# Performance work log

Hardware: AMD Instinct MI355X
Metric: run time of the kernel (lower is better)

## Reference

```python
import jax, jax.numpy as jnp
import numpy as np

B, S, H, NH = 4, 2048, 256, 8
EPS = 1e-5


def setup_inputs() -> dict:
    key = jax.random.key(0)
    ks = jax.random.split(key, 12)
    p = lambda k, shape: (jax.random.normal(k, shape, jnp.float32) * 0.02)
    return {
        "x": jax.random.normal(ks[0], (B, S, H), jnp.float32),
        "lengths": jax.random.randint(ks[1], (B,), 0, S).astype(jnp.int32),
        "atten_in": jnp.zeros((1,), jnp.float32),
        "Wq": p(ks[2], (H, H)), "bq": jnp.zeros((H,), jnp.float32),
        "Wk": p(ks[3], (H, H)), "bk": jnp.zeros((H,), jnp.float32),
        "Wv": p(ks[4], (H, H)), "bv": jnp.zeros((H,), jnp.float32),
        "W1": p(ks[5], (H, H)), "b1": jnp.zeros((H,), jnp.float32),
        "W2": p(ks[6], (H, H)), "b2": jnp.zeros((H,), jnp.float32),
        "g1": jnp.ones((H,), jnp.float32), "beta1": jnp.zeros((H,), jnp.float32),
        "g2": jnp.ones((H,), jnp.float32), "beta2": jnp.zeros((H,), jnp.float32),
    }


def _layer_norm(x, g, b):
    mu = x.mean(-1, keepdims=True)
    var = ((x - mu) ** 2).mean(-1, keepdims=True)
    return (x - mu) / jnp.sqrt(var + EPS) * g + b


def reference(x, lengths, atten_in, Wq, bq, Wk, bk, Wv, bv, W1, b1, W2, b2, g1, beta1, g2, beta2):
    Bx, Sx, Hx = x.shape
    hd = Hx // NH
    # QKV projections, split heads -> [B, NH, S, hd]
    q = (x @ Wq + bq).reshape(Bx, Sx, NH, hd).transpose(0, 2, 1, 3)
    k = (x @ Wk + bk).reshape(Bx, Sx, NH, hd).transpose(0, 2, 1, 3)
    v = (x @ Wv + bv).reshape(Bx, Sx, NH, hd).transpose(0, 2, 1, 3)
    # NOTE: original scales by sqrt(hidden_size), not sqrt(head_dim)
    scores = jnp.einsum('bhqd,bhkd->bhqk', q, k) / np.sqrt(Hx).astype(np.float32)
    pos = jnp.arange(Sx)
    causal = pos[:, None] >= pos[None, :]                     # [S, S]
    row_ok = pos[None, :] < lengths[:, None]                  # [B, S]: mask query rows >= length
    head_ok = jnp.arange(NH)[None, :] < lengths[:, None]      # [B, NH]: original loop masks heads >= length
    mask = causal[None, None] & row_ok[:, None, :, None] & head_ok[:, :, None, None]
    neg = jnp.finfo(scores.dtype).min
    logits = jnp.where(mask, scores, neg)
    atten = jax.nn.softmax(logits, axis=-1)
    # original: masked_fill((atten > 0) == False, 0) -> fully masked rows (NaN in torch) become 0
    atten = jnp.where(mask, atten, 0.0)
    row_valid = mask.any(-1, keepdims=True)
    atten = jnp.where(row_valid, atten, 0.0)
    out = jnp.einsum('bhqk,bhkd->bhqd', atten, v).transpose(0, 2, 1, 3).reshape(Bx, Sx, Hx)
    atten_mean = atten.mean(axis=1)  # [B, S, S], detached in original
    out_1 = x + out  # dropout p=0 / eval mode -> identity
    out_1_norm = _layer_norm(out_1, g1, beta1)
    ff = jax.nn.gelu(out_1_norm @ W1 + b1, approximate=False) @ W2 + b2
    y_prim = _layer_norm(out_1_norm + ff, g2, beta2)
    return (y_prim, lengths, atten_mean)
```

## Files before the change

### kernel.cpp

```cpp
#include <hip/hip_runtime.h>
#include <math.h>

#define BB 4
#define SS 2048
#define HH 256
#define NHH 8
#define EPSV 1e-5f
#define NC 8
#define CHW (SS/NC)
#define NCO 4
#define QPRE 0.09016844005556021f

#if __has_builtin(__builtin_amdgcn_exp2f)
#define EXP2F(x) __builtin_amdgcn_exp2f(x)
#else
#define EXP2F(x) __expf((x) * 0.6931471805599453f)
#endif

typedef unsigned short ushortT;
typedef __attribute__((ext_vector_type(8))) short bf16x8;
typedef __attribute__((ext_vector_type(4))) float f32x4;

__device__ inline ushortT f2bf(float f) {
    union { float f; unsigned int u; } x; x.f = f;
    unsigned int r = x.u + 0x7FFFu + ((x.u >> 16) & 1u);
    return (ushortT)(r >> 16);
}
__device__ inline ushortT f2bf_rz(float f) {
    union { float f; unsigned int u; } x; x.f = f;
    return (ushortT)(x.u >> 16);
}
__device__ inline float bf2f(ushortT u) {
    union { unsigned int i; float f; } x; x.i = ((unsigned int)u) << 16;
    return x.f;
}

__global__ __launch_bounds__(256) void prep(const int* __restrict__ L,
        float* __restrict__ out_len,
        const float* __restrict__ Wa, const float* __restrict__ Wb,
        const float* __restrict__ Wc, const float* __restrict__ Wd,
        const float* __restrict__ We, ushortT* __restrict__ Wtb) {
    const int wb = blockIdx.x;
    if (wb == 0 && threadIdx.x < BB) out_len[threadIdx.x] = (float)L[threadIdx.x];
    const int z = wb >> 6;
    const int rem = wb & 63;
    const int k0 = (rem >> 3) << 5, n0 = (rem & 7) << 5;
    const float* W = (z == 0) ? Wa : (z == 1) ? Wb : (z == 2) ? Wc : (z == 3) ? Wd : We;
    __shared__ float tile[32][33];
    const int t = threadIdx.x;
    const int r = t >> 3, c4 = (t & 7) << 2;
    float4 v = *(const float4*)(W + (size_t)(k0 + r) * HH + n0 + c4);
    tile[r][c4+0] = v.x; tile[r][c4+1] = v.y; tile[r][c4+2] = v.z; tile[r][c4+3] = v.w;
    __syncthreads();
    ushort4 o;
    o.x = f2bf(tile[c4+0][r]); o.y = f2bf(tile[c4+1][r]);
    o.z = f2bf(tile[c4+2][r]); o.w = f2bf(tile[c4+3][r]);
    *(ushort4*)(Wtb + (size_t)z * 65536 + (size_t)(n0 + r) * HH + k0 + c4) = o;
}

__global__ __launch_bounds__(256) void gemm_qkv(const float* __restrict__ X,
        const ushortT* __restrict__ Wtb,
        const float* __restrict__ bq, const float* __restrict__ bk,
        const float* __restrict__ bv,
        ushortT* __restrict__ Qb, ushortT* __restrict__ Kb,
        ushortT* __restrict__ Vt) {
    __shared__ ushortT As[64][264];
    __shared__ ushortT Ws[64][264];
    const int wsel = blockIdx.y >> 2;
    const int n0 = (blockIdx.y & 3) << 6;
    const ushortT* Wt = Wtb + (size_t)wsel * 65536;
    const float* bias = (wsel == 0) ? bq : (wsel == 1) ? bk : bv;
    const int tid = threadIdx.x;
    const int m0 = blockIdx.x << 6;
    #pragma unroll
    for (int t = 0; t < 8; ++t) {
        const int f = t * 256 + tid;
        const int r = f >> 5;
        const int cc = (f & 31) << 3;
        const float* xrow = X + (size_t)(m0 + r) * HH + cc;
        float4 v0 = *(const float4*)xrow;
        float4 v1 = *(const float4*)(xrow + 4);
        bf16x8 o;
        o[0] = (short)f2bf(v0.x); o[1] = (short)f2bf(v0.y);
        o[2] = (short)f2bf(v0.z); o[3] = (short)f2bf(v0.w);
        o[4] = (short)f2bf(v1.x); o[5] = (short)f2bf(v1.y);
        o[6] = (short)f2bf(v1.z); o[7] = (short)f2bf(v1.w);
        *(bf16x8*)&As[r][cc] = o;
        *(bf16x8*)&Ws[r][cc] = *(const bf16x8*)(Wt + (size_t)(n0 + r) * HH + cc);
    }
    __syncthreads();
    const int w = tid >> 6, lane = tid & 63;
    const int lg = lane >> 4, lc = lane & 15;
    const int wr = (w & 1) << 5, wc = (w >> 1) << 5;
    f32x4 acc[2][2];
    const f32x4 z4 = {0.f, 0.f, 0.f, 0.f};
    acc[0][0] = z4; acc[0][1] = z4; acc[1][0] = z4; acc[1][1] = z4;
    #pragma unroll
    for (int k0 = 0; k0 < 256; k0 += 32) {
        bf16x8 a0 = *(const bf16x8*)&As[wr + lc][k0 + lg*8];
        bf16x8 a1 = *(const bf16x8*)&As[wr + 16 + lc][k0 + lg*8];
        bf16x8 b0 = *(const bf16x8*)&Ws[wc + lc][k0 + lg*8];
        bf16x8 b1 = *(const bf16x8*)&Ws[wc + 16 + lc][k0 + lg*8];
        acc[0][0] = __builtin_amdgcn_mfma_f32_16x16x32_bf16(a0, b0, acc[0][0], 0, 0, 0);
        acc[0][1] = __builtin_amdgcn_mfma_f32_16x16x32_bf16(a0, b1, acc[0][1], 0, 0, 0);
        acc[1][0] = __builtin_amdgcn_mfma_f32_16x16x32_bf16(a1, b0, acc[1][0], 0, 0, 0);
        acc[1][1] = __builtin_amdgcn_mfma_f32_16x16x32_bf16(a1, b1, acc[1][1], 0, 0, 0);
    }
    ushortT* Out = (wsel == 0) ? Qb : Kb;
    #pragma unroll
    for (int RH = 0; RH < 2; ++RH)
        #pragma unroll
        for (int CH = 0; CH < 2; ++CH) {
            const int col = n0 + wc + CH*16 + lc;
            const float bvv = bias[col];
            float v[4];
            #pragma unroll
            for (int r = 0; r < 4; ++r) {
                v[r] = acc[RH][CH][r] + bvv;
                if (wsel == 0) v[r] *= QPRE;
            }
            if (wsel < 2) {
                #pragma unroll
                for (int r = 0; r < 4; ++r) {
                    const int row = m0 + wr + RH*16 + lg*4 + r;
                    Out[(size_t)row * HH + col] = f2bf(v[r]);
                }
            } else {
                const int row0 = m0 + wr + RH*16 + lg*4;
                const int bidx = row0 >> 11, s0 = row0 & (SS - 1);
                ushort4 o;
                o.x = f2bf(v[0]); o.y = f2bf(v[1]); o.z = f2bf(v[2]); o.w = f2bf(v[3]);
                *(ushort4*)(Vt + ((size_t)(bidx * HH + col)) * SS + s0) = o;
            }
        }
}

template<int MODE>
__global__ __launch_bounds__(256) void gemm_mfma(const ushortT* __restrict__ A,
        const ushortT* __restrict__ Wt, const float* __restrict__ bias,
        void* __restrict__ Cv) {
    __shared__ ushortT As[64][264];
    __shared__ ushortT Ws[64][264];
    const int tid = threadIdx.x;
    const int m0 = blockIdx.x << 6;
    const int n0 = blockIdx.y << 6;
    #pragma unroll
    for (int t = 0; t < 8; ++t) {
        const int f = t * 256 + tid;
        const int r = f >> 5;
        const int cc = (f & 31) << 3;
        *(bf16x8*)&As[r][cc] = *(const bf16x8*)(A + (size_t)(m0 + r) * HH + cc);
        *(bf16x8*)&Ws[r][cc] = *(const bf16x8*)(Wt + (size_t)(n0 + r) * HH + cc);
    }
    __syncthreads();
    const int w = tid >> 6, lane = tid & 63;
    const int lg = lane >> 4, lc = lane & 15;
    const int wr = (w & 1) << 5, wc = (w >> 1) << 5;
    f32x4 acc[2][2];
    const f32x4 z4 = {0.f, 0.f, 0.f, 0.f};
    acc[0][0] = z4; acc[0][1] = z4; acc[1][0] = z4; acc[1][1] = z4;
    #pragma unroll
    for (int k0 = 0; k0 < 256; k0 += 32) {
        bf16x8 a0 = *(const bf16x8*)&As[wr + lc][k0 + lg*8];
        bf16x8 a1 = *(const bf16x8*)&As[wr + 16 + lc][k0 + lg*8];
        bf16x8 b0 = *(const bf16x8*)&Ws[wc + lc][k0 + lg*8];
        bf16x8 b1 = *(const bf16x8*)&Ws[wc + 16 + lc][k0 + lg*8];
        acc[0][0] = __builtin_amdgcn_mfma_f32_16x16x32_bf16(a0, b0, acc[0][0], 0, 0, 0);
        acc[0][1] = __builtin_amdgcn_mfma_f32_16x16x32_bf16(a0, b1, acc[0][1], 0, 0, 0);
        acc[1][0] = __builtin_amdgcn_mfma_f32_16x16x32_bf16(a1, b0, acc[1][0], 0, 0, 0);
        acc[1][1] = __builtin_amdgcn_mfma_f32_16x16x32_bf16(a1, b1, acc[1][1], 0, 0, 0);
    }
    #pragma unroll
    for (int RH = 0; RH < 2; ++RH)
        #pragma unroll
        for (int CH = 0; CH < 2; ++CH) {
            const int col = n0 + wc + CH*16 + lc;
            const float bv = bias[col];
            #pragma unroll
            for (int r = 0; r < 4; ++r) {
                const int row = m0 + wr + RH*16 + lg*4 + r;
                float v = acc[RH][CH][r] + bv;
                if (MODE == 2) v = 0.5f * v * (1.0f + erff(v * 0.70710678118f));
                ((ushortT*)Cv)[(size_t)row * HH + col] = f2bf(v);
            }
        }
}

__global__ __launch_bounds__(512) void ffn2_ln(const ushortT* __restrict__ A,
        const ushortT* __restrict__ W2t, const float* __restrict__ b2,
        const float* __restrict__ X1N, const float* __restrict__ g,
        const float* __restrict__ be, float* __restrict__ out) {
    __shared__ ushortT Ws[256][264];
    __shared__ ushortT As[32][264];
    __shared__ float redA[8][32];
    __shared__ float redB[8][32];
    const int tid = threadIdx.x;
    const int m0 = blockIdx.x << 5;
    #pragma unroll
    for (int t = 0; t < 16; ++t) {
        const int f = t * 512 + tid;
        const int r = f >> 5;
        const int cc = (f & 31) << 3;
        *(bf16x8*)&Ws[r][cc] = *(const bf16x8*)(W2t + (size_t)r * HH + cc);
    }
    #pragma unroll
    for (int t = 0; t < 2; ++t) {
        const int f = t * 512 + tid;
        const int r = f >> 5;
        const int cc = (f & 31) << 3;
        *(bf16x8*)&As[r][cc] = *(const bf16x8*)(A + (size_t)(m0 + r) * HH + cc);
    }
    __syncthreads();
    const int w = tid >> 6, lane = tid & 63;
    const int lg = lane >> 4, lc = lane & 15;
    const int n0 = (w >> 1) << 6;
    const int ch = (w & 1) << 5;
    f32x4 acc[2][2];
    const f32x4 z4 = {0.f, 0.f, 0.f, 0.f};
    acc[0][0] = z4; acc[0][1] = z4; acc[1][0] = z4; acc[1][1] = z4;
    #pragma unroll
    for (int k0 = 0; k0 < 256; k0 += 32) {
        bf16x8 a0 = *(const bf16x8*)&As[lc][k0 + lg*8];
        bf16x8 a1 = *(const bf16x8*)&As[16 + lc][k0 + lg*8];
        bf16x8 b0 = *(const bf16x8*)&Ws[n0 + ch + lc][k0 + lg*8];
        bf16x8 b1 = *(const bf16x8*)&Ws[n0 + ch + 16 + lc][k0 + lg*8];
        acc[0][0] = __builtin_amdgcn_mfma_f32_16x16x32_bf16(a0, b0, acc[0][0], 0, 0, 0);
        acc[0][1] = __builtin_amdgcn_mfma_f32_16x16x32_bf16(a0, b1, acc[0][1], 0, 0, 0);
        acc[1][0] = __builtin_amdgcn_mfma_f32_16x16x32_bf16(a1, b0, acc[1][0], 0, 0, 0);
        acc[1][1] = __builtin_amdgcn_mfma_f32_16x16x32_bf16(a1, b1, acc[1][1], 0, 0, 0);
    }
    float v[2][2][4];
    float rs[2][4] = {};
    #pragma unroll
    for (int RH = 0; RH < 2; ++RH)
        #pragma unroll
        for (int CH = 0; CH < 2; ++CH) {
            const int col = n0 + ch + CH*16 + lc;
            const float bv = b2[col];
            #pragma unroll
            for (int r = 0; r < 4; ++r) {
                const int row = m0 + RH*16 + lg*4 + r;
                float vv = acc[RH][CH][r] + bv + X1N[(size_t)row * HH + col];
                v[RH][CH][r] = vv;
                rs[RH][r] += vv;
            }
        }
    #pragma unroll
    for (int RH = 0; RH < 2; ++RH)
        #pragma unroll
        for (int r = 0; r < 4; ++r) {
            rs[RH][r] += __shfl_xor(rs[RH][r], 1);
            rs[RH][r] += __shfl_xor(rs[RH][r], 2);
            rs[RH][r] += __shfl_xor(rs[RH][r], 4);
            rs[RH][r] += __shfl_xor(rs[RH][r], 8);
        }
    if (lc == 0) {
        #pragma unroll
        for (int RH = 0; RH < 2; ++RH)
            #pragma unroll
            for (int r = 0; r < 4; ++r)
                redA[w][RH*16 + lg*4 + r] = rs[RH][r];
    }
    __syncthreads();
    float mu[2][4];
    #pragma unroll
    for (int RH = 0; RH < 2; ++RH)
        #pragma unroll
        for (int r = 0; r < 4; ++r) {
            const int rl = RH*16 + lg*4 + r;
            mu[RH][r] = (redA[0][rl] + redA[1][rl] + redA[2][rl] + redA[3][rl]
                       + redA[4][rl] + redA[5][rl] + redA[6][rl] + redA[7][rl])
                      * 0.00390625f;
        }
    float qs[2][4] = {};
    #pragma unroll
    for (int RH = 0; RH < 2; ++RH)
        #pragma unroll
        for (int CH = 0; CH < 2; ++CH)
            #pragma unroll
            for (int r = 0; r < 4; ++r) {
                const float d = v[RH][CH][r] - mu[RH][r];
                qs[RH][r] += d * d;
            }
    #pragma unroll
    for (int RH = 0; RH < 2; ++RH)
        #pragma unroll
        for (int r = 0; r < 4; ++r) {
            qs[RH][r] += __shfl_xor(qs[RH][r], 1);
            qs[RH][r] += __shfl_xor(qs[RH][r], 2);
            qs[RH][r] += __shfl_xor(qs[RH][r], 4);
            qs[RH][r] += __shfl_xor(qs[RH][r], 8);
        }
    if (lc == 0) {
        #pragma unroll
        for (int RH = 0; RH < 2; ++RH)
            #pragma unroll
            for (int r = 0; r < 4; ++r)
                redB[w][RH*16 + lg*4 + r] = qs[RH][r];
    }
    __syncthreads();
    #pragma unroll
    for (int RH = 0; RH < 2; ++RH)
        #pragma unroll
        for (int r = 0; r < 4; ++r) {
            const int rl = RH*16 + lg*4 + r;
            const float var = (redB[0][rl] + redB[1][rl] + redB[2][rl] + redB[3][rl]
                             + redB[4][rl] + redB[5][rl] + redB[6][rl] + redB[7][rl])
                            * 0.00390625f;
            const float rq = rsqrtf(var + EPSV);
            const int row = m0 + rl;
            #pragma unroll
            for (int CH = 0; CH < 2; ++CH) {
                const int col = n0 + ch + CH*16 + lc;
                out[(size_t)row * HH + col] =
                    (v[RH][CH][r] - mu[RH][r]) * rq * g[col] + be[col];
            }
        }
}

__global__ __launch_bounds__(512) void attn_sums(const ushortT* __restrict__ Qb,
        const ushortT* __restrict__ Kb, const int* __restrict__ lengths,
        float* __restrict__ Psum, float* __restrict__ out_mean) {
    const int b = blockIdx.z, c = blockIdx.y;
    const int i0 = (63 - blockIdx.x) << 5;
    const int len = lengths[b];
    const int tid = threadIdx.x;
    const int w = tid >> 6, lane = tid & 63;
    const int T = (i0 < len) ? ((min(i0 + 31, len - 1) >> 5) + 1) : 0;
    {
        const int zs = max(T * 32 - c * CHW, 0);
        if (zs < CHW) {
            #pragma unroll
            for (int rr = 0; rr < 4; ++rr) {
                float* mrow = out_mean + ((size_t)(b * SS + i0 + w * 4 + rr)) * SS + c * CHW;
                const int col = zs + (lane << 2);
                if (col < CHW)
                    *(float4*)(mrow + col) = make_float4(0.f, 0.f, 0.f, 0.f);
            }
        }
    }
    const int jmax = min(i0 + 31, len - 1);
    const int jstart = c * CHW;
    if (i0 >= len || jstart > jmax) return;
    const int lg = lane >> 4, lc = lane & 15;
    bf16x8 qf[2];
    #pragma unroll
    for (int RH = 0; RH < 2; ++RH)
        qf[RH] = *(const bf16x8*)(Qb + ((size_t)(b * SS + i0 + RH*16 + lc)) * HH + w*32 + lg*8);
    const f32x4 z4 = {0.f, 0.f, 0.f, 0.f};
    float lsum[2][4] = {};
    const int jend = min(jstart + CHW - 32, (jmax >> 5) << 5);
    bf16x8 kf0 = *(const bf16x8*)(Kb + ((size_t)(b * SS + jstart + lc)) * HH + w*32 + lg*8);
    bf16x8 kf1 = *(const bf16x8*)(Kb + ((size_t)(b * SS + jstart + 16 + lc)) * HH + w*32 + lg*8);
    for (int j0 = jstart; j0 <= jend; j0 += 32) {
        bf16x8 ck0 = kf0, ck1 = kf1;
        if (j0 + 32 <= jend) {
            kf0 = *(const bf16x8*)(Kb + ((size_t)(b * SS + j0 + 32 + lc)) * HH + w*32 + lg*8);
            kf1 = *(const bf16x8*)(Kb + ((size_t)(b * SS + j0 + 48 + lc)) * HH + w*32 + lg*8);
        }
        f32x4 s[2][2];
        #pragma unroll
        for (int RH = 0; RH < 2; ++RH) {
            s[RH][0] = __builtin_amdgcn_mfma_f32_16x16x32_bf16(qf[RH], ck0, z4, 0, 0, 0);
            s[RH][1] = __builtin_amdgcn_mfma_f32_16x16x32_bf16(qf[RH], ck1, z4, 0, 0, 0);
        }
        if (j0 < i0) {
            #pragma unroll
            for (int RH = 0; RH < 2; ++RH)
                #pragma unroll
                for (int r = 0; r < 4; ++r)
                    #pragma unroll
                    for (int CH = 0; CH < 2; ++CH)
                        lsum[RH][r] += EXP2F(s[RH][CH][r]);
        } else {
            #pragma unroll
            for (int RH = 0; RH < 2; ++RH)
                #pragma unroll
                for (int r = 0; r < 4; ++r) {
                    const int row = i0 + RH*16 + lg*4 + r;
                    #pragma unroll
                    for (int CH = 0; CH < 2; ++CH) {
                        const int j = j0 + CH*16 + lc;
                        lsum[RH][r] += (j <= row) ? EXP2F(s[RH][CH][r]) : 0.f;
                    }
                }
        }
    }
    #pragma unroll
    for (int RH = 0; RH < 2; ++RH)
        #pragma unroll
        for (int r = 0; r < 4; ++r) {
            float v = lsum[RH][r];
            v += __shfl_xor(v, 1); v += __shfl_xor(v, 2);
            v += __shfl_xor(v, 4); v += __shfl_xor(v, 8);
            if (lc == 0)
                Psum[((size_t)(c * BB + b) * NHH + w) * SS + i0 + RH*16 + lg*4 + r] = v;
        }
}

__global__ __launch_bounds__(512) void attn_pv(const ushortT* __restrict__ Qb,
        const ushortT* __restrict__ Kb, const ushortT* __restrict__ Vt,
        const int* __restrict__ lengths, const float* __restrict__ Psum,
        ushortT* __restrict__ OPart, float* __restrict__ out_mean) {
    __shared__ __align__(16) ushortT Pb[2][NHH][32][40];
    __shared__ float invS[NHH][32];
    const int b = blockIdx.z, cg = blockIdx.y;
    const int i0 = (63 - blockIdx.x) << 5;
    const int len = lengths[b];
    const int tid = threadIdx.x;
    const int mr = tid >> 4, mc = (tid & 15) << 1;
    float* meanrow = out_mean + ((size_t)(b * SS + i0 + mr)) * SS + mc;
    const int T = (i0 < len) ? ((min(i0 + 31, len - 1) >> 5) + 1) : 0;
    const int q = T >> 2, r = T & (NCO - 1);
    const int t0 = cg * q + min(cg, r);
    const int t1 = t0 + q + (cg < r ? 1 : 0);
    if (t0 >= t1) return;
    if (tid < NHH * 32) {
        const int hh = tid >> 5, row = i0 + (tid & 31);
        float rv = 0.f;
        if (row < len && hh < len) {
            float s = 0.f;
            const int ncv = (row >> 8) + 1;
            for (int c2 = 0; c2 < ncv; ++c2)
                s += Psum[((size_t)(c2 * BB + b) * NHH + hh) * SS + row];
            rv = (s > 0.f) ? 1.0f / s : 0.f;
        }
        invS[hh][tid & 31] = rv;
    }
    __syncthreads();
    const int w = tid >> 6, lane = tid & 63;
    const int lg = lane >> 4, lc = lane & 15;
    bf16x8 qf[2];
    #pragma unroll
    for (int RH = 0; RH < 2; ++RH)
        qf[RH] = *(const bf16x8*)(Qb + ((size_t)(b * SS + i0 + RH*16 + lc)) * HH + w*32 + lg*8);
    float invv[2][4];
    #pragma unroll
    for (int RH = 0; RH < 2; ++RH)
        #pragma unroll
        for (int r2 = 0; r2 < 4; ++r2)
            invv[RH][r2] = invS[w][RH*16 + lg*4 + r2];
    float invh8[NHH];
    #pragma unroll
    for (int hh = 0; hh < NHH; ++hh)
        invh8[hh] = invS[hh][mr] * 0.125f;
    const f32x4 z4 = {0.f, 0.f, 0.f, 0.f};
    f32x4 O[2][2];
    O[0][0] = z4; O[0][1] = z4; O[1][0] = z4; O[1][1] = z4;
    const int jstart = t0 << 5;
    bf16x8 kf0 = *(const bf16x8*)(Kb + ((size_t)(b * SS + jstart + lc)) * HH + w*32 + lg*8);
    bf16x8 kf1 = *(const bf16x8*)(Kb + ((size_t)(b * SS + jstart + 16 + lc)) * HH + w*32 + lg*8);
    bf16x8 vf0 = *(const bf16x8*)(Vt + ((size_t)(b * HH + w*32 + lc)) * SS + jstart + lg*8);
    bf16x8 vf1 = *(const bf16x8*)(Vt + ((size_t)(b * HH + w*32 + 16 + lc)) * SS + jstart + lg*8);
    for (int t = t0; t < t1; ++t) {
        const int j0 = t << 5;
        const int par = t & 1;
        bf16x8 ck0 = kf0, ck1 = kf1, cv0 = vf0, cv1 = vf1;
        if (t + 1 < t1) {
            kf0 = *(const bf16x8*)(Kb + ((size_t)(b * SS + j0 + 32 + lc)) * HH + w*32 + lg*8);
            kf1 = *(const bf16x8*)(Kb + ((size_t)(b * SS + j0 + 48 + lc)) * HH + w*32 + lg*8);
            vf0 = *(const bf16x8*)(Vt + ((size_t)(b * HH + w*32 + lc)) * SS + j0 + 32 + lg*8);
            vf1 = *(const bf16x8*)(Vt + ((size_t)(b * HH + w*32 + 16 + lc)) * SS + j0 + 32 + lg*8);
        }
        f32x4 s[2][2];
        #pragma unroll
        for (int RH = 0; RH < 2; ++RH) {
            s[RH][0] = __builtin_amdgcn_mfma_f32_16x16x32_bf16(qf[RH], ck0, z4, 0, 0, 0);
            s[RH][1] = __builtin_amdgcn_mfma_f32_16x16x32_bf16(qf[RH], ck1, z4, 0, 0, 0);
        }
        if (j0 < i0) {
            #pragma unroll
            for (int RH = 0; RH < 2; ++RH)
                #pragma unroll
                for (int CH = 0; CH < 2; ++CH)
                    #pragma unroll
                    for (int r2 = 0; r2 < 4; ++r2)
                        Pb[par][w][RH*16 + lg*4 + r2][CH*16 + lc] =
                            f2bf_rz(EXP2F(s[RH][CH][r2]));
        } else {
            #pragma unroll
            for (int RH = 0; RH < 2; ++RH)
                #pragma unroll
                for (int CH = 0; CH < 2; ++CH)
                    #pragma unroll
                    for (int r2 = 0; r2 < 4; ++r2) {
                        const int row = i0 + RH*16 + lg*4 + r2;
                        const int j = j0 + CH*16 + lc;
                        Pb[par][w][RH*16 + lg*4 + r2][CH*16 + lc] =
                            (j <= row) ? f2bf_rz(EXP2F(s[RH][CH][r2])) : (ushortT)0;
                    }
        }
        #pragma unroll
        for (int RH = 0; RH < 2; ++RH) {
            bf16x8 pa = *(const bf16x8*)&Pb[par][w][RH*16 + lc][lg*8];
            O[RH][0] = __builtin_amdgcn_mfma_f32_16x16x32_bf16(pa, cv0, O[RH][0], 0, 0, 0);
            O[RH][1] = __builtin_amdgcn_mfma_f32_16x16x32_bf16(pa, cv1, O[RH][1], 0, 0, 0);
        }
        __syncthreads();
        float m0 = 0.f, m1 = 0.f;
        #pragma unroll
        for (int ww = 0; ww < NHH; ++ww) {
            ushort2 t2 = *(const ushort2*)&Pb[par][ww][mr][mc];
            m0 += bf2f(t2.x) * invh8[ww]; m1 += bf2f(t2.y) * invh8[ww];
        }
        *(float2*)(meanrow + j0) = make_float2(m0, m1);
    }
    ushortT* op = OPart + (size_t)cg * ((size_t)BB * SS * HH);
    #pragma unroll
    for (int RH = 0; RH < 2; ++RH)
        #pragma unroll
        for (int DH = 0; DH < 2; ++DH)
            #pragma unroll
            for (int r2 = 0; r2 < 4; ++r2)
                op[((size_t)(b * SS + i0 + RH*16 + lg*4 + r2)) * HH + w*32 + DH*16 + lc] =
                    f2bf(O[RH][DH][r2] * invv[RH][r2]);
}

__global__ __launch_bounds__(256) void add_ln_attn(const float* __restrict__ x,
        const ushortT* __restrict__ OPart, const int* __restrict__ lengths,
        const float* __restrict__ g, const float* __restrict__ beta,
        float* __restrict__ out, ushortT* __restrict__ outb) {
    const int row = blockIdx.x;
    const int c = threadIdx.x;
    const int i = row & (SS - 1);
    const int len = lengths[row >> 11];
    const size_t base = (size_t)row * 256;
    float v = x[base + c];
    if (i < len) {
        const int ncv = min(NCO, (i >> 5) + 1);
        for (int cc = 0; cc < ncv; ++cc)
            v += bf2f(OPart[(size_t)cc * ((size_t)BB * SS * HH) + base + c]);
    }
    __shared__ float red[8];
    float s = v;
    #pragma unroll
    for (int o = 32; o; o >>= 1) s += __shfl_down(s, o, 64);
    const int wid = c >> 6, lane = c & 63;
    if (lane == 0) red[wid] = s;
    __syncthreads();
    float mu = (red[0] + red[1] + red[2] + red[3]) * 0.00390625f;
    float d = v - mu;
    float q = d * d;
    #pragma unroll
    for (int o = 32; o; o >>= 1) q += __shfl_down(q, o, 64);
    if (lane == 0) red[4 + wid] = q;
    __syncthreads();
    float var = (red[4] + red[5] + red[6] + red[7]) * 0.00390625f;
    float res = d * rsqrtf(var + EPSV) * g[c] + beta[c];
    out[base + c] = res;
    outb[base + c] = f2bf(res);
}

extern "C" void kernel_launch(void* const* d_in, const int* in_sizes, int n_in,
                              void* d_out, int out_size, void* d_ws, size_t ws_size,
                              hipStream_t stream) {
    const float* x   = (const float*)d_in[0];
    const int* lengths = (const int*)d_in[1];
    const float* Wq  = (const float*)d_in[3];
    const float* bq  = (const float*)d_in[4];
    const float* Wk  = (const float*)d_in[5];
    const float* bk  = (const float*)d_in[6];
    const float* Wv  = (const float*)d_in[7];
    const float* bv  = (const float*)d_in[8];
    const float* W1  = (const float*)d_in[9];
    const float* b1  = (const float*)d_in[10];
    const float* W2  = (const float*)d_in[11];
    const float* b2  = (const float*)d_in[12];
    const float* g1  = (const float*)d_in[13];
    const float* be1 = (const float*)d_in[14];
    const float* g2  = (const float*)d_in[15];
    const float* be2 = (const float*)d_in[16];
    float* out = (float*)d_out;
    float* ws  = (float*)d_ws;

    const size_t NELT = (size_t)BB * SS * HH;
    const size_t M1 = 1024 * 1024;

    float*   Psum = ws;
    ushortT* Qbf = (ushortT*)(ws + M1);
    ushortT* Kbf = (ushortT*)(ws + 2 * M1);
    ushortT* Vtb = (ushortT*)(ws + 3 * M1);
    float*   X1N  = ws + 4 * M1;
    ushortT* Wtb = (ushortT*)(ws + 6 * M1);
    ushortT* OPart = (ushortT*)(ws + 7 * M1);
    ushortT* X1Nb = (ushortT*)ws;
    ushortT* F1b  = (ushortT*)(ws + M1);

    float* out_y    = out;
    float* out_len  = out + NELT;
    float* out_mean = out + NELT + 4;

    prep<<<320, 256, 0, stream>>>(lengths, out_len, Wq, Wk, Wv, W1, W2, Wtb);
    gemm_qkv<<<dim3(128, 12), 256, 0, stream>>>(x, Wtb, bq, bk, bv, Qbf, Kbf, Vtb);
    attn_sums<<<dim3(64, NC, 4), 512, 0, stream>>>(Qbf, Kbf, lengths, Psum, out_mean);
    attn_pv<<<dim3(64, NCO, 4), 512, 0, stream>>>(Qbf, Kbf, Vtb, lengths, Psum, OPart, out_mean);
    add_ln_attn<<<8192, 256, 0, stream>>>(x, OPart, lengths, g1, be1, X1N, X1Nb);
    gemm_mfma<2><<<dim3(128, 4), 256, 0, stream>>>(X1Nb, Wtb + 3 * 65536, b1, (void*)F1b);
    ffn2_ln<<<256, 512, 0, stream>>>(F1b, Wtb + 4 * 65536, b2, X1N, g2, be2, out_y);
}
```

Baseline: 97.97 us.

## Fuse residual-add LayerNorm into the first FFN GEMM kernel

Replaces the separate add_ln_attn kernel and the gemm_mfma<2> FFN1 kernel with a single ln_ffn1 kernel. Each 512-thread block computes the LayerNorm for 32 rows, writes the bf16 result directly into shared memory, and multiplies it by the full W1 held in LDS, applying bias and GELU. This removes one launch and the global round-trip of the bf16 normalized activations. In exchange, each block reloads the whole 256x256 W1 into about 135KB of LDS, and the grid drops to 256 blocks, which reduces parallelism and occupancy.

```diff
diff --git a/kernel.cpp b/kernel.cpp
--- a/kernel.cpp
+++ b/kernel.cpp
@@ -135,36 +135,73 @@
         }
 }
 
-template<int MODE>
-__global__ __launch_bounds__(256) void gemm_mfma(const ushortT* __restrict__ A,
-        const ushortT* __restrict__ Wt, const float* __restrict__ bias,
-        void* __restrict__ Cv) {
-    __shared__ ushortT As[64][264];
-    __shared__ ushortT Ws[64][264];
+__global__ __launch_bounds__(512) void ln_ffn1(const float* __restrict__ x,
+        const ushortT* __restrict__ OPart, const int* __restrict__ lengths,
+        const float* __restrict__ g, const float* __restrict__ beta,
+        const ushortT* __restrict__ W1t, const float* __restrict__ b1,
+        float* __restrict__ X1N, ushortT* __restrict__ F1b) {
+    __shared__ ushortT Ws[256][264];
+    __shared__ ushortT As[32][264];
     const int tid = threadIdx.x;
-    const int m0 = blockIdx.x << 6;
-    const int n0 = blockIdx.y << 6;
-    #pragma unroll
-    for (int t = 0; t < 8; ++t) {
-        const int f = t * 256 + tid;
+    const int m0 = blockIdx.x << 5;
+    #pragma unroll
+    for (int t = 0; t < 16; ++t) {
+        const int f = t * 512 + tid;
         const int r = f >> 5;
         const int cc = (f & 31) << 3;
-        *(bf16x8*)&As[r][cc] = *(const bf16x8*)(A + (size_t)(m0 + r) * HH + cc);
-        *(bf16x8*)&Ws[r][cc] = *(const bf16x8*)(Wt + (size_t)(n0 + r) * HH + cc);
-    }
-    __syncthreads();
+        *(bf16x8*)&Ws[r][cc] = *(const bf16x8*)(W1t + (size_t)r * HH + cc);
+    }
     const int w = tid >> 6, lane = tid & 63;
     const int lg = lane >> 4, lc = lane & 15;
-    const int wr = (w & 1) << 5, wc = (w >> 1) << 5;
+    const int len = lengths[m0 >> 11];
+    const int col0 = lane << 2;
+    #pragma unroll
+    for (int rr = 0; rr < 4; ++rr) {
+        const int row = m0 + w * 4 + rr;
+        const int i = row & (SS - 1);
+        const size_t base = (size_t)row * HH;
+        float4 v = *(const float4*)(x + base + col0);
+        if (i < len) {
+            const int ncv = min(NCO, (i >> 5) + 1);
+            for (int cc = 0; cc < ncv; ++cc) {
+                ushort4 o = *(const ushort4*)(OPart +
+                    (size_t)cc * ((size_t)BB * SS * HH) + base + col0);
+                v.x += bf2f(o.x); v.y += bf2f(o.y);
+                v.z += bf2f(o.z); v.w += bf2f(o.w);
+            }
+        }
+        float s = v.x + v.y + v.z + v.w;
+        #pragma unroll
+        for (int o = 1; o < 64; o <<= 1) s += __shfl_xor(s, o);
+        const float mu = s * 0.00390625f;
+        float4 d = make_float4(v.x - mu, v.y - mu, v.z - mu, v.w - mu);
+        float q = d.x*d.x + d.y*d.y + d.z*d.z + d.w*d.w;
+        #pragma unroll
+        for (int o = 1; o < 64; o <<= 1) q += __shfl_xor(q, o);
+        const float rs = rsqrtf(q * 0.00390625f + EPSV);
+        float4 res;
+        res.x = d.x * rs * g[col0+0] + beta[col0+0];
+        res.y = d.y * rs * g[col0+1] + beta[col0+1];
+        res.z = d.z * rs * g[col0+2] + beta[col0+2];
+        res.w = d.w * rs * g[col0+3] + beta[col0+3];
+        *(float4*)(X1N + base + col0) = res;
+        ushort4 rb;
+        rb.x = f2bf(res.x); rb.y = f2bf(res.y);
+        rb.z = f2bf(res.z); rb.w = f2bf(res.w);
+        *(ushort4*)&As[w * 4 + rr][col0] = rb;
+    }
+    __syncthreads();
+    const int n0 = (w >> 1) << 6;
+    const int ch = (w & 1) << 5;
     f32x4 acc[2][2];
     const f32x4 z4 = {0.f, 0.f, 0.f, 0.f};
     acc[0][0] = z4; acc[0][1] = z4; acc[1][0] = z4; acc[1][1] = z4;
     #pragma unroll
     for (int k0 = 0; k0 < 256; k0 += 32) {
-        bf16x8 a0 = *(const bf16x8*)&As[wr + lc][k0 + lg*8];
-        bf16x8 a1 = *(const bf16x8*)&As[wr + 16 + lc][k0 + lg*8];
-        bf16x8 b0 = *(const bf16x8*)&Ws[wc + lc][k0 + lg*8];
-        bf16x8 b1 = *(const bf16x8*)&Ws[wc + 16 + lc][k0 + lg*8];
+        bf16x8 a0 = *(const bf16x8*)&As[lc][k0 + lg*8];
+        bf16x8 a1 = *(const bf16x8*)&As[16 + lc][k0 + lg*8];
+        bf16x8 b0 = *(const bf16x8*)&Ws[n0 + ch + lc][k0 + lg*8];
+        bf16x8 b1 = *(const bf16x8*)&Ws[n0 + ch + 16 + lc][k0 + lg*8];
         acc[0][0] = __builtin_amdgcn_mfma_f32_16x16x32_bf16(a0, b0, acc[0][0], 0, 0, 0);
         acc[0][1] = __builtin_amdgcn_mfma_f32_16x16x32_bf16(a0, b1, acc[0][1], 0, 0, 0);
         acc[1][0] = __builtin_amdgcn_mfma_f32_16x16x32_bf16(a1, b0, acc[1][0], 0, 0, 0);
@@ -174,14 +211,14 @@
     for (int RH = 0; RH < 2; ++RH)
         #pragma unroll
         for (int CH = 0; CH < 2; ++CH) {
-            const int col = n0 + wc + CH*16 + lc;
-            const float bv = bias[col];
+            const int col = n0 + ch + CH*16 + lc;
+            const float bv = b1[col];
             #pragma unroll
             for (int r = 0; r < 4; ++r) {
-                const int row = m0 + wr + RH*16 + lg*4 + r;
+                const int row = m0 + RH*16 + lg*4 + r;
                 float v = acc[RH][CH][r] + bv;
-                if (MODE == 2) v = 0.5f * v * (1.0f + erff(v * 0.70710678118f));
-                ((ushortT*)Cv)[(size_t)row * HH + col] = f2bf(v);
+                v = 0.5f * v * (1.0f + erff(v * 0.70710678118f));
+                F1b[(size_t)row * HH + col] = f2bf(v);
             }
         }
 }
@@ -516,41 +553,6 @@
                     f2bf(O[RH][DH][r2] * invv[RH][r2]);
 }
 
-__global__ __launch_bounds__(256) void add_ln_attn(const float* __restrict__ x,
-        const ushortT* __restrict__ OPart, const int* __restrict__ lengths,
-        const float* __restrict__ g, const float* __restrict__ beta,
-        float* __restrict__ out, ushortT* __restrict__ outb) {
-    const int row = blockIdx.x;
-    const int c = threadIdx.x;
-    const int i = row & (SS - 1);
-    const int len = lengths[row >> 11];
-    const size_t base = (size_t)row * 256;
-    float v = x[base + c];
-    if (i < len) {
-        const int ncv = min(NCO, (i >> 5) + 1);
-        for (int cc = 0; cc < ncv; ++cc)
-            v += bf2f(OPart[(size_t)cc * ((size_t)BB * SS * HH) + base + c]);
-    }
-    __shared__ float red[8];
-    float s = v;
-    #pragma unroll
-    for (int o = 32; o; o >>= 1) s += __shfl_down(s, o, 64);
-    const int wid = c >> 6, lane = c & 63;
-    if (lane == 0) red[wid] = s;
-    __syncthreads();
-    float mu = (red[0] + red[1] + red[2] + red[3]) * 0.00390625f;
-    float d = v - mu;
-    float q = d * d;
-    #pragma unroll
-    for (int o = 32; o; o >>= 1) q += __shfl_down(q, o, 64);
-    if (lane == 0) red[4 + wid] = q;
-    __syncthreads();
-    float var = (red[4] + red[5] + red[6] + red[7]) * 0.00390625f;
-    float res = d * rsqrtf(var + EPSV) * g[c] + beta[c];
-    out[base + c] = res;
-    outb[base + c] = f2bf(res);
-}
-
 extern "C" void kernel_launch(void* const* d_in, const int* in_sizes, int n_in,
                               void* d_out, int out_size, void* d_ws, size_t ws_size,
                               hipStream_t stream) {
@@ -583,7 +585,6 @@
     float*   X1N  = ws + 4 * M1;
     ushortT* Wtb = (ushortT*)(ws + 6 * M1);
     ushortT* OPart = (ushortT*)(ws + 7 * M1);
-    ushortT* X1Nb = (ushortT*)ws;
     ushortT* F1b  = (ushortT*)(ws + M1);
 
     float* out_y    = out;
@@ -594,7 +595,7 @@
     gemm_qkv<<<dim3(128, 12), 256, 0, stream>>>(x, Wtb, bq, bk, bv, Qbf, Kbf, Vtb);
     attn_sums<<<dim3(64, NC, 4), 512, 0, stream>>>(Qbf, Kbf, lengths, Psum, out_mean);
     attn_pv<<<dim3(64, NCO, 4), 512, 0, stream>>>(Qbf, Kbf, Vtb, lengths, Psum, OPart, out_mean);
-    add_ln_attn<<<8192, 256, 0, stream>>>(x, OPart, lengths, g1, be1, X1N, X1Nb);
-    gemm_mfma<2><<<dim3(128, 4), 256, 0, stream>>>(X1Nb, Wtb + 3 * 65536, b1, (void*)F1b);
+    ln_ffn1<<<256, 512, 0, stream>>>(x, OPart, lengths, g1, be1,
+                                     Wtb + 3 * 65536, b1, X1N, F1b);
     ffn2_ln<<<256, 512, 0, stream>>>(F1b, Wtb + 4 * 65536, b2, X1N, g2, be2, out_y);
 }
```

Result: faster. 94.87 us (-3.2%).
